# Performance work log

Hardware: AMD Instinct MI355X
Metric: run time of the kernel (lower is better)

Reference implementation:

```python
import jax, jax.numpy as jnp
import numpy as np

SCALING = 32.0 / 16.0  # alpha / rank

def setup_inputs() -> dict:
    key = jax.random.key(0)
    k1, k2, k3, k4 = jax.random.split(key, 4)
    B_, S, D_in, D_out, R = 4, 4096, 2048, 2048, 16
    x = jax.random.normal(k1, (B_, S, D_in), dtype=jnp.float32)
    # dequantized 4-bit base weight, torch Linear layout [out, in]
    W_base = jax.random.normal(k2, (D_out, D_in), dtype=jnp.float32) * 0.02
    A = jax.random.normal(k3, (R, D_in), dtype=jnp.float32) * (1.0 / np.sqrt(D_in))
    # torch code zero-inits lora_B, but use random for nontrivial gradient checking
    B = jax.random.normal(k4, (D_out, R), dtype=jnp.float32) * 0.02
    return {"x": x, "W_base": W_base, "A": A, "B": B}

def reference(x, W_base, A, B):
    # base: Y = x @ W_base^T   [b, s, out]
    base = jnp.einsum('bsd,od->bso', x, W_base)
    # LoRA: (x @ A^T) @ B^T * scaling   (rank is tiny, keep factored)
    lora = jnp.einsum('bsr,or->bso', jnp.einsum('bsd,rd->bsr', x, A), B)
    return base + lora * SCALING
```

## Files before the change

kernel.cpp:

```cpp
#include <hip/hip_runtime.h>


typedef __bf16 bf16x8 __attribute__((ext_vector_type(8)));
typedef float  f32x4  __attribute__((ext_vector_type(4)));
typedef unsigned short u16x8 __attribute__((ext_vector_type(8)));

#define AS1C(p) ((const __attribute__((address_space(1))) void*)(p))
#define AS3(p)  ((__attribute__((address_space(3))) void*)(p))

__device__ __forceinline__ unsigned short f2bf_rne(float f) {
  unsigned int u = __float_as_uint(f);
  u += 0x7FFFu + ((u >> 16) & 1u);
  return (unsigned short)(u >> 16);
}

constexpr int M_ = 16384;
constexpr int N_ = 2048;
constexpr int K_ = 2048;
constexpr int R_ = 16;
constexpr float SCALING = 2.0f;

constexpr int BM = 256, BN = 256, BK = 64;
constexpr int NT = K_ / BK;

__global__ __launch_bounds__(256) void cvt_kernel(const float* __restrict__ in,
                                                  unsigned short* __restrict__ out) {
  size_t i = (size_t)blockIdx.x * blockDim.x + threadIdx.x;
  const float4* p = (const float4*)in;
  float4 a = p[2 * i];
  float4 b = p[2 * i + 1];
  u16x8 o;
  o[0] = f2bf_rne(a.x); o[1] = f2bf_rne(a.y); o[2] = f2bf_rne(a.z); o[3] = f2bf_rne(a.w);
  o[4] = f2bf_rne(b.x); o[5] = f2bf_rne(b.y); o[6] = f2bf_rne(b.z); o[7] = f2bf_rne(b.w);
  ((u16x8*)out)[i] = o;
}

__global__ __launch_bounds__(256) void weff_kernel(const float* __restrict__ W,
                                                   const float* __restrict__ A,
                                                   const float* __restrict__ Bl,
                                                   unsigned short* __restrict__ out) {
  int idx = blockIdx.x * blockDim.x + threadIdx.x;
  int o = idx >> 11;
  int d = idx & 2047;
  float acc = W[idx];
#pragma unroll
  for (int r = 0; r < R_; ++r)
    acc = fmaf(SCALING * Bl[o * R_ + r], A[r * K_ + d], acc);
  out[idx] = f2bf_rne(acc);
}

__global__ __launch_bounds__(512, 2) void gemm_kernel(const unsigned short* __restrict__ X,
                                                      const unsigned short* __restrict__ W,
                                                      float* __restrict__ C) {
  __shared__ __align__(16) unsigned short sA[2][BM * BK];
  __shared__ __align__(16) unsigned short sB[2][BN * BK];

  const int tid  = threadIdx.x;
  const int w    = tid >> 6;
  const int lane = tid & 63;
  const int fm   = lane & 15;
  const int quad = lane >> 4;

  const int id = blockIdx.x;
  const int bm = ((id & 7) * 8 + (id >> 6)) * BM;
  const int bn = ((id >> 3) & 7) * BN;

  const int wrow = (w >> 2) * 128;
  const int wcol = (w & 3) * 64;

  const int strow = tid >> 3;
  const int gseg  = ((tid & 7) - strow) & 7;
  const int brow0 = 64 * (tid >> 8) + (strow & 31);

  const unsigned short* xa = X + (size_t)(bm + strow) * K_ + gseg * 8;
  const unsigned short* xb = W + (size_t)(bn + brow0) * K_ + gseg * 8;

  const int aw = w * 8 * BK;
  const int bw = ((w >> 2) * 64 + (w & 3) * 8) * BK;

  const int sp0 = ((quad + fm) & 7) * 8;
  const int sp1 = ((quad + fm + 4) & 7) * 8;

  f32x4 acc[8][4] = {};

#define STAGE_A(hm, kt, b) do {                                                   \
    __builtin_amdgcn_global_load_lds(AS1C(xa + (size_t)((hm) * 64) * K_ + (kt) * BK), \
        AS3(&sA[b][((hm) * 64) * BK + aw]), 16, 0, 0);                            \
    __builtin_amdgcn_global_load_lds(AS1C(xa + (size_t)((hm) * 64 + 128) * K_ + (kt) * BK), \
        AS3(&sA[b][((hm) * 64 + 128) * BK + aw]), 16, 0, 0);                      \
  } while (0)

#define STAGE_B(hn, kt, b) do {                                                   \
    __builtin_amdgcn_global_load_lds(AS1C(xb + (size_t)((hn) * 32) * K_ + (kt) * BK), \
        AS3(&sB[b][((hn) * 32) * BK + bw]), 16, 0, 0);                            \
    __builtin_amdgcn_global_load_lds(AS1C(xb + (size_t)((hn) * 32 + 128) * K_ + (kt) * BK), \
        AS3(&sB[b][((hn) * 32 + 128) * BK + bw]), 16, 0, 0);                      \
  } while (0)

#define VMC4 asm volatile("s_waitcnt vmcnt(4)" ::: "memory")
#define NOVM (void)0

#define PHASE(tb, hm, hn, STAGE, VMW) do {                                        \
    bf16x8 af[4][2], bv[2][2];                                                    \
    _Pragma("unroll")                                                             \
    for (int i2 = 0; i2 < 4; ++i2) {                                              \
      const int ra = (wrow + (hm) * 64 + i2 * 16 + fm) * BK;                      \
      af[i2][0] = *(const bf16x8*)&sA[tb][ra + sp0];                              \
      af[i2][1] = *(const bf16x8*)&sA[tb][ra + sp1];                              \
    }                                                                             \
    _Pragma("unroll")                                                             \
    for (int j2 = 0; j2 < 2; ++j2) {                                              \
      const int rb = (wcol + (hn) * 32 + j2 * 16 + fm) * BK;                      \
      bv[j2][0] = *(const bf16x8*)&sB[tb][rb + sp0];                              \
      bv[j2][1] = *(const bf16x8*)&sB[tb][rb + sp1];                              \
    }                                                                             \
    STAGE;                                                                        \
    __builtin_amdgcn_s_barrier();                                                 \
    asm volatile("s_waitcnt lgkmcnt(0)" ::: "memory");                            \
    __builtin_amdgcn_s_setprio(1);                                                \
    _Pragma("unroll")                                                             \
    for (int ks = 0; ks < 2; ++ks)                                                \
      _Pragma("unroll")                                                           \
      for (int i2 = 0; i2 < 4; ++i2)                                              \
        _Pragma("unroll")                                                         \
        for (int j2 = 0; j2 < 2; ++j2)                                            \
          acc[(hm) * 4 + i2][(hn) * 2 + j2] = __builtin_amdgcn_mfma_f32_16x16x32_bf16( \
              af[i2][ks], bv[j2][ks], acc[(hm) * 4 + i2][(hn) * 2 + j2], 0, 0, 0); \
    __builtin_amdgcn_s_setprio(0);                                                \
    VMW;                                                                          \
    __builtin_amdgcn_s_barrier();                                                 \
  } while (0)

  STAGE_B(0, 0, 0);
  STAGE_A(0, 0, 0);
  STAGE_A(1, 0, 0);
  STAGE_B(1, 0, 0);
  STAGE_B(0, 1, 1);
  STAGE_A(0, 1, 1);
  asm volatile("s_waitcnt vmcnt(4)" ::: "memory");
  __builtin_amdgcn_s_barrier();

#pragma unroll 1
  for (int it = 0; it < NT / 2; ++it) {
    const int t1 = 2 * it + 1;
    const int t2 = (2 * it + 2 < NT) ? 2 * it + 2 : NT - 1;
    const int t3 = (2 * it + 3 < NT) ? 2 * it + 3 : NT - 1;
    PHASE(0, 0, 0, STAGE_A(1, t1, 1), NOVM);
    PHASE(0, 1, 0, STAGE_B(1, t1, 1), NOVM);
    PHASE(0, 0, 1, STAGE_B(0, t2, 0), NOVM);
    PHASE(0, 1, 1, STAGE_A(0, t2, 0), VMC4);
    PHASE(1, 0, 0, STAGE_A(1, t2, 0), NOVM);
    PHASE(1, 1, 0, STAGE_B(1, t2, 0), NOVM);
    PHASE(1, 0, 1, STAGE_B(0, t3, 1), NOVM);
    PHASE(1, 1, 1, STAGE_A(0, t3, 1), VMC4);
  }

  asm volatile("s_waitcnt vmcnt(0)" ::: "memory");

  const int r0 = quad * 4;
#pragma unroll
  for (int i = 0; i < 8; ++i) {
#pragma unroll
    for (int j = 0; j < 4; ++j) {
      size_t base = (size_t)(bm + wrow + i * 16 + r0) * N_ + (size_t)(bn + wcol + j * 16 + fm);
#pragma unroll
      for (int r = 0; r < 4; ++r)
        __builtin_nontemporal_store(acc[i][j][r], &C[base + (size_t)r * N_]);
    }
  }
#undef PHASE
#undef STAGE_A
#undef STAGE_B
#undef VMC4
#undef NOVM
}

extern "C" void kernel_launch(void* const* d_in, const int* in_sizes, int n_in,
                              void* d_out, int out_size, void* d_ws, size_t ws_size,
                              hipStream_t stream) {
  const float* x  = (const float*)d_in[0];
  const float* W  = (const float*)d_in[1];
  const float* A  = (const float*)d_in[2];
  const float* Bl = (const float*)d_in[3];
  float* out = (float*)d_out;

  unsigned short* Xb   = (unsigned short*)d_ws;
  unsigned short* Weff = Xb + (size_t)M_ * K_;

  cvt_kernel<<<(int)((size_t)M_ * K_ / 8 / 256), 256, 0, stream>>>(x, Xb);
  weff_kernel<<<(N_ * K_) / 256, 256, 0, stream>>>(W, A, Bl, Weff);

  gemm_kernel<<<(M_ / BM) * (N_ / BN), 512, 0, stream>>>(Xb, Weff, out);
}
```

Before: 403.7 us.

## Reorder GEMM quadrants in snake order to reuse A/B fragments across phases

```diff
diff --git a/kernel.cpp b/kernel.cpp
--- a/kernel.cpp
+++ b/kernel.cpp
@@ -82,6 +82,9 @@
   const int sp1 = ((quad + fm + 4) & 7) * 8;
 
   f32x4 acc[8][4] = {};
+  bf16x8 af[4][2];
+  bf16x8 bv0[2][2];
+  bf16x8 bv1[2][2];
 
 #define STAGE_A(hm, kt, b) do {                                                   \
     __builtin_amdgcn_global_load_lds(AS1C(xa + (size_t)((hm) * 64) * K_ + (kt) * BK), \
@@ -97,26 +100,25 @@
         AS3(&sB[b][((hn) * 32 + 128) * BK + bw]), 16, 0, 0);                      \
   } while (0)
 
-#define VMC4 asm volatile("s_waitcnt vmcnt(4)" ::: "memory")
-#define NOVM (void)0
-
-#define PHASE(tb, hm, hn, STAGE, VMW) do {                                        \
-    bf16x8 af[4][2], bv[2][2];                                                    \
+#define LOAD_A(hm, tb) do {                                                       \
     _Pragma("unroll")                                                             \
     for (int i2 = 0; i2 < 4; ++i2) {                                              \
       const int ra = (wrow + (hm) * 64 + i2 * 16 + fm) * BK;                      \
       af[i2][0] = *(const bf16x8*)&sA[tb][ra + sp0];                              \
       af[i2][1] = *(const bf16x8*)&sA[tb][ra + sp1];                              \
     }                                                                             \
+  } while (0)
+
+#define LOAD_B(bv, hn, tb) do {                                                   \
     _Pragma("unroll")                                                             \
     for (int j2 = 0; j2 < 2; ++j2) {                                              \
       const int rb = (wcol + (hn) * 32 + j2 * 16 + fm) * BK;                      \
       bv[j2][0] = *(const bf16x8*)&sB[tb][rb + sp0];                              \
       bv[j2][1] = *(const bf16x8*)&sB[tb][rb + sp1];                              \
     }                                                                             \
-    STAGE;                                                                        \
-    __builtin_amdgcn_s_barrier();                                                 \
-    asm volatile("s_waitcnt lgkmcnt(0)" ::: "memory");                            \
+  } while (0)
+
+#define MFMA_Q(hm, hn, bv) do {                                                   \
     __builtin_amdgcn_s_setprio(1);                                                \
     _Pragma("unroll")                                                             \
     for (int ks = 0; ks < 2; ++ks)                                                \
@@ -125,34 +127,53 @@
         _Pragma("unroll")                                                         \
         for (int j2 = 0; j2 < 2; ++j2)                                            \
           acc[(hm) * 4 + i2][(hn) * 2 + j2] = __builtin_amdgcn_mfma_f32_16x16x32_bf16( \
-              af[i2][ks], bv[j2][ks], acc[(hm) * 4 + i2][(hn) * 2 + j2], 0, 0, 0); \
+              af[i2][ks], (bv)[j2][ks], acc[(hm) * 4 + i2][(hn) * 2 + j2], 0, 0, 0); \
     __builtin_amdgcn_s_setprio(0);                                                \
-    VMW;                                                                          \
-    __builtin_amdgcn_s_barrier();                                                 \
-  } while (0)
-
+  } while (0)
+
+#define PH_BAR __builtin_amdgcn_s_barrier()
+#define LGKM0  asm volatile("s_waitcnt lgkmcnt(0)" ::: "memory")
+#define VMC6   asm volatile("s_waitcnt vmcnt(6)" ::: "memory")
+
+  STAGE_A(0, 0, 0);
   STAGE_B(0, 0, 0);
-  STAGE_A(0, 0, 0);
+  STAGE_B(1, 0, 0);
   STAGE_A(1, 0, 0);
-  STAGE_B(1, 0, 0);
+  STAGE_A(0, 1, 1);
   STAGE_B(0, 1, 1);
-  STAGE_A(0, 1, 1);
-  asm volatile("s_waitcnt vmcnt(4)" ::: "memory");
-  __builtin_amdgcn_s_barrier();
+  STAGE_B(1, 1, 1);
+  VMC6;
+  PH_BAR;
 
 #pragma unroll 1
   for (int it = 0; it < NT / 2; ++it) {
     const int t1 = 2 * it + 1;
     const int t2 = (2 * it + 2 < NT) ? 2 * it + 2 : NT - 1;
     const int t3 = (2 * it + 3 < NT) ? 2 * it + 3 : NT - 1;
-    PHASE(0, 0, 0, STAGE_A(1, t1, 1), NOVM);
-    PHASE(0, 1, 0, STAGE_B(1, t1, 1), NOVM);
-    PHASE(0, 0, 1, STAGE_B(0, t2, 0), NOVM);
-    PHASE(0, 1, 1, STAGE_A(0, t2, 0), VMC4);
-    PHASE(1, 0, 0, STAGE_A(1, t2, 0), NOVM);
-    PHASE(1, 1, 0, STAGE_B(1, t2, 0), NOVM);
-    PHASE(1, 0, 1, STAGE_B(0, t3, 1), NOVM);
-    PHASE(1, 1, 1, STAGE_A(0, t3, 1), VMC4);
+
+    LOAD_A(0, 0); LOAD_B(bv0, 0, 0);
+    STAGE_A(1, t1, 1);
+    PH_BAR; LGKM0; MFMA_Q(0, 0, bv0); PH_BAR;
+    LOAD_B(bv1, 1, 0);
+    STAGE_A(0, t2, 0);
+    PH_BAR; LGKM0; MFMA_Q(0, 1, bv1); PH_BAR;
+    LOAD_A(1, 0);
+    STAGE_B(0, t2, 0);
+    PH_BAR; LGKM0; MFMA_Q(1, 1, bv1); PH_BAR;
+    STAGE_B(1, t2, 0);
+    PH_BAR; MFMA_Q(1, 0, bv0); VMC6; PH_BAR;
+
+    LOAD_A(0, 1); LOAD_B(bv0, 0, 1);
+    STAGE_A(1, t2, 0);
+    PH_BAR; LGKM0; MFMA_Q(0, 0, bv0); PH_BAR;
+    LOAD_B(bv1, 1, 1);
+    STAGE_A(0, t3, 1);
+    PH_BAR; LGKM0; MFMA_Q(0, 1, bv1); PH_BAR;
+    LOAD_A(1, 1);
+    STAGE_B(0, t3, 1);
+    PH_BAR; LGKM0; MFMA_Q(1, 1, bv1); PH_BAR;
+    STAGE_B(1, t3, 1);
+    PH_BAR; MFMA_Q(1, 0, bv0); VMC6; PH_BAR;
   }
 
   asm volatile("s_waitcnt vmcnt(0)" ::: "memory");
@@ -168,11 +189,14 @@
         __builtin_nontemporal_store(acc[i][j][r], &C[base + (size_t)r * N_]);
     }
   }
-#undef PHASE
+#undef PH_BAR
+#undef LGKM0
+#undef VMC6
+#undef MFMA_Q
+#undef LOAD_A
+#undef LOAD_B
 #undef STAGE_A
 #undef STAGE_B
-#undef VMC4
-#undef NOVM
 }
 
 extern "C" void kernel_launch(void* const* d_in, const int* in_sizes, int n_in,
```

New measurement: 379.9 us. 1.06x faster.
